# Kernel optimization log

Hardware: AMD Instinct MI355X
Metric: run time of the kernel (lower is better)

Reference implementation:

```python
import jax, jax.numpy as jnp
import numpy as np
from jax import lax

# quantization constants (from init_kwargs)
IN_SCALE = 0.05
IN_ZP = 128
W_SCALE = 0.02
W_ZP = 128
OUT_SCALE = 0.1
OUT_ZP = 0
PADDING = 1


def setup_inputs() -> dict:
    key = jax.random.key(0)
    k1, k2, k3 = jax.random.split(key, 3)
    x_float = jax.random.normal(k1, (8, 32, 512, 512), dtype=jnp.float32)
    weight = jax.random.randint(k2, (32, 32, 3, 3), 0, 256, dtype=jnp.int32)  # uint8-like
    bias = jax.random.randint(k3, (32,), 0, 100, dtype=jnp.int32)  # int32 accumulator bias
    return {"x_float": x_float, "weight": weight, "bias": bias}


def reference(x_float, weight, bias):
    # quantize input to uint8 range, then recenter
    x_q = jnp.round(x_float / IN_SCALE) + IN_ZP
    x_q = jnp.clip(x_q, 0, 255).astype(jnp.int32) - IN_ZP
    # recenter weights
    w_q = weight - W_ZP
    # integer conv emulated in float (NCHW, OIHW), 'same' padding=1
    y_int = lax.conv_general_dilated(
        x_q.astype(jnp.float32), w_q.astype(jnp.float32),
        window_strides=(1, 1), padding=[(PADDING, PADDING), (PADDING, PADDING)],
        dimension_numbers=("NCHW", "OIHW", "NCHW"),
    ).astype(jnp.int32)
    y_int = y_int + bias[None, :, None, None]
    # requantize + dequantize + relu (fused elementwise)
    scale_float = IN_SCALE * W_SCALE / OUT_SCALE
    y_q = jnp.clip(jnp.round(y_int.astype(jnp.float32) * scale_float), -127, 127).astype(jnp.int32)
    y = (y_q - OUT_ZP).astype(jnp.float32) * OUT_SCALE
    return jax.nn.relu(y)
```

## Files before the change

kernel.cpp:

```cpp
#include <hip/hip_runtime.h>


#define N_IMG 8
#define CIN   32
#define COUT  32
#define HD    512
#define WD    512
#define PH    514
#define PW    514
#define TH    8

typedef int intx4 __attribute__((ext_vector_type(4)));
typedef short short8 __attribute__((ext_vector_type(8)));
typedef float floatx4 __attribute__((ext_vector_type(4)));

#define XQ_BYTES ((size_t)N_IMG * PH * PW * CIN)
#define SLACK    256
#define WP_BYTES (6 * 32 * 64)
#define WS_NEED  (XQ_BYTES + SLACK + WP_BYTES)

__global__ __launch_bounds__(256) void quant8_kernel(const float* __restrict__ x,
                                                     unsigned char* __restrict__ xq) {
    const int gid = blockIdx.x * 256 + threadIdx.x;
    const int w = gid & (WD - 1);
    const int h = (gid >> 9) & (HD - 1);
    const int n = gid >> 18;
    const float* xp = x + ((size_t)n * CIN * HD + h) * WD + w;
    unsigned int pk[8];
#pragma unroll
    for (int c = 0; c < CIN; c += 4) {
        unsigned int b[4];
#pragma unroll
        for (int j = 0; j < 4; ++j) {
            float xv = xp[(size_t)(c + j) * (HD * WD)];
            float q = rintf(xv / 0.05f);
            q = fminf(fmaxf(q, -128.0f), 127.0f);
            b[j] = (unsigned int)(int)q & 0xffu;
        }
        pk[c >> 2] = b[0] | (b[1] << 8) | (b[2] << 16) | (b[3] << 24);
    }
    uint4* dst = (uint4*)(xq + (((size_t)n * PH + h + 1) * PW + (w + 1)) * CIN);
    dst[0] = make_uint4(pk[0], pk[1], pk[2], pk[3]);
    dst[1] = make_uint4(pk[4], pk[5], pk[6], pk[7]);
}

#define N_BORDER (N_IMG * 2052)
#define N_WP     (6 * 32 * 64)
__global__ __launch_bounds__(256) void aux8_kernel(const int* __restrict__ wq,
                                                   unsigned char* __restrict__ xq,
                                                   char* __restrict__ wp) {
    const int gid = blockIdx.x * 256 + threadIdx.x;
    if (gid < N_BORDER) {
        const int n = gid / 2052;
        const int p = gid - n * 2052;
        int h, w;
        if (p < 514)       { h = 0;   w = p; }
        else if (p < 1028) { h = 513; w = p - 514; }
        else { int q = p - 1028; h = 1 + (q >> 1); w = (q & 1) ? 513 : 0; }
        uint4* dst = (uint4*)(xq + (((size_t)n * PH + h) * PW + w) * CIN);
        uint4 z = make_uint4(0u, 0u, 0u, 0u);
        dst[0] = z; dst[1] = z;
    } else if (gid < N_BORDER + N_WP) {
        const int i = gid - N_BORDER;
        const int row  = i >> 6;
        const int k    = i & 63;
        const int khp  = row >> 5;
        const int cout = row & 31;
        const int kh   = khp >> 1;
        const int pr   = khp & 1;
        const int sel  = k >> 5;
        const int cin  = k & 31;
        const int kw   = pr * 2 + sel;
        int val = 0;
        if (kw < 3) val = wq[((cout * CIN + cin) * 3 + kh) * 3 + kw] - 128;
        wp[i] = (char)val;
    }
}

__global__ __launch_bounds__(256, 3) void conv8_kernel(const unsigned char* __restrict__ xq,
                                                       const char* __restrict__ wp,
                                                       const int* __restrict__ bias,
                                                       float* __restrict__ out) {
    const int tid  = threadIdx.x;
    const int lane = tid & 63;
    const int wave = tid >> 6;
    const int l15  = lane & 15;
    const int quad = lane >> 4;
    const int bx = blockIdx.x;
    const int by = blockIdx.y;
    const int n  = blockIdx.z;

    intx4 Af[3][2][2];
#pragma unroll
    for (int kh = 0; kh < 3; ++kh)
#pragma unroll
        for (int p = 0; p < 2; ++p)
#pragma unroll
            for (int hf = 0; hf < 2; ++hf)
                Af[kh][p][hf] = *(const intx4*)(wp + (((kh * 2 + p) * 32 + hf * 16 + l15) << 6) + quad * 16);

    int bi0[4], bi1[4];
#pragma unroll
    for (int r = 0; r < 4; ++r) { bi0[r] = bias[quad * 4 + r]; bi1[r] = bias[16 + quad * 4 + r]; }

    const int w0 = bx * 64 + wave * 16;
    const size_t rstride = (size_t)PW * CIN;
    const unsigned char* pbase = xq + (((size_t)n * PH + by * TH) * PW + (w0 + l15)) * CIN + quad * 16;

    intx4 Bf[10][2];
#pragma unroll
    for (int r = 0; r < 4; ++r)
#pragma unroll
        for (int p = 0; p < 2; ++p)
            Bf[r][p] = *(const intx4*)(pbase + r * rstride + p * 64);

#pragma unroll
    for (int it = 0; it < 4; ++it) {
        if (it < 3) {
#pragma unroll
            for (int r = 0; r < 2; ++r)
#pragma unroll
                for (int p = 0; p < 2; ++p)
                    Bf[2 * it + 4 + r][p] = *(const intx4*)(pbase + (2 * it + 4 + r) * rstride + p * 64);
        }
        intx4 acc[2][2];
#pragma unroll
        for (int o = 0; o < 2; ++o)
#pragma unroll
            for (int hf = 0; hf < 2; ++hf)
                acc[o][hf] = (intx4){0, 0, 0, 0};
#pragma unroll
        for (int o = 0; o < 2; ++o)
#pragma unroll
            for (int kh = 0; kh < 3; ++kh)
#pragma unroll
                for (int p = 0; p < 2; ++p) {
                    const intx4 b = Bf[2 * it + o + kh][p];
                    acc[o][0] = __builtin_amdgcn_mfma_i32_16x16x64_i8(Af[kh][p][0], b, acc[o][0], 0, 0, 0);
                    acc[o][1] = __builtin_amdgcn_mfma_i32_16x16x64_i8(Af[kh][p][1], b, acc[o][1], 0, 0, 0);
                }
#pragma unroll
        for (int o = 0; o < 2; ++o) {
            const int h = by * TH + 2 * it + o;
            float* op0 = out + (((size_t)n * COUT + quad * 4) * HD + h) * WD + w0 + l15;
            float* op1 = op0 + (size_t)16 * HD * WD;
#pragma unroll
            for (int r = 0; r < 4; ++r) {
                int v0 = acc[o][0][r] + bi0[r];
                float yq0 = rintf((float)v0 * 0.01f);
                yq0 = fminf(fmaxf(yq0, -127.f), 127.f);
                op0[(size_t)r * (HD * WD)] = fmaxf(yq0 * 0.1f, 0.f);
                int v1 = acc[o][1][r] + bi1[r];
                float yq1 = rintf((float)v1 * 0.01f);
                yq1 = fminf(fmaxf(yq1, -127.f), 127.f);
                op1[(size_t)r * (HD * WD)] = fmaxf(yq1 * 0.1f, 0.f);
            }
        }
    }
}

__launch_bounds__(256, 2)
__global__ void conv2d_int8_fused(const float* __restrict__ x,
                                  const int* __restrict__ wq,
                                  const int* __restrict__ bias,
                                  float* __restrict__ out)
{
    __shared__ unsigned short xs[10 * 66 * 32];
    __shared__ unsigned short ws[9 * 32 * 32];
    const int tid = threadIdx.x;
    const int bx = blockIdx.x, by = blockIdx.y, n = blockIdx.z;
    for (int i = tid; i < COUT * CIN * 9; i += 256) {
        int cout = i / 288, rem = i - cout * 288, cin = rem / 9, t = rem - cin * 9;
        float f = (float)(wq[i] - 128);
        ws[(t * 32 + cout) * 32 + cin] = (unsigned short)(__float_as_uint(f) >> 16);
    }
    const int h_base = by * TH - 1;
    const int w_base = bx * 64 - 1;
    for (int j = tid; j < CIN * 10 * 66; j += 256) {
        int c = j / 660, rem = j - c * 660, r = rem / 66, wc = rem - r * 66;
        int h = h_base + r, w = w_base + wc;
        float q = 0.0f;
        if ((unsigned)h < (unsigned)HD && (unsigned)w < (unsigned)WD) {
            float xv = x[((size_t)(n * CIN + c) * HD + h) * WD + w];
            q = rintf(xv / 0.05f);
            q = fminf(fmaxf(q, -128.0f), 127.0f);
        }
        unsigned short b = (unsigned short)(__float_as_uint(q) >> 16);
        int pix = r * 66 + wc;
        int grp = (c >> 3) ^ (pix & 3);
        xs[pix * 32 + (grp << 3) + (c & 7)] = b;
    }
    __syncthreads();
    const int lane = tid & 63, wave = tid >> 6;
    const int l15 = lane & 15, quad = lane >> 4;
    short8 bfrag[9][2];
#pragma unroll
    for (int t = 0; t < 9; ++t)
#pragma unroll
        for (int hf = 0; hf < 2; ++hf)
            bfrag[t][hf] = *(const short8*)&ws[(t * 32 + hf * 16 + l15) * 32 + quad * 8];
    const float b0 = (float)bias[l15];
    const float b1 = (float)bias[16 + l15];
    const int wseg = wave * 16;
    for (int hr = 0; hr < TH; ++hr) {
        floatx4 acc0 = {0.f, 0.f, 0.f, 0.f};
        floatx4 acc1 = {0.f, 0.f, 0.f, 0.f};
#pragma unroll
        for (int kh = 0; kh < 3; ++kh)
#pragma unroll
            for (int kw = 0; kw < 3; ++kw) {
                int pix = (hr + kh) * 66 + wseg + l15 + kw;
                int grp = quad ^ (pix & 3);
                short8 a = *(const short8*)&xs[pix * 32 + (grp << 3)];
                int t = kh * 3 + kw;
                acc0 = __builtin_amdgcn_mfma_f32_16x16x32_bf16(a, bfrag[t][0], acc0, 0, 0, 0);
                acc1 = __builtin_amdgcn_mfma_f32_16x16x32_bf16(a, bfrag[t][1], acc1, 0, 0, 0);
            }
        const int h_out = by * TH + hr;
        const int w_out0 = bx * 64 + wseg;
#pragma unroll
        for (int r = 0; r < 4; ++r) {
            int wo = w_out0 + quad * 4 + r;
            {
                float v = acc0[r] + b0;
                float yq = rintf(v * 0.01f);
                yq = fminf(fmaxf(yq, -127.f), 127.f);
                out[((size_t)(n * COUT + l15) * HD + h_out) * WD + wo] = fmaxf(yq * 0.1f, 0.f);
            }
            {
                float v = acc1[r] + b1;
                float yq = rintf(v * 0.01f);
                yq = fminf(fmaxf(yq, -127.f), 127.f);
                out[((size_t)(n * COUT + 16 + l15) * HD + h_out) * WD + wo] = fmaxf(yq * 0.1f, 0.f);
            }
        }
    }
}

extern "C" void kernel_launch(void* const* d_in, const int* in_sizes, int n_in,
                              void* d_out, int out_size, void* d_ws, size_t ws_size,
                              hipStream_t stream) {
    const float* x  = (const float*)d_in[0];
    const int*   wq = (const int*)d_in[1];
    const int*   bi = (const int*)d_in[2];
    float* out = (float*)d_out;

    if (ws_size >= WS_NEED) {
        unsigned char* xq = (unsigned char*)d_ws;
        char* wp = (char*)d_ws + XQ_BYTES + SLACK;
        aux8_kernel<<<(N_BORDER + N_WP + 255) / 256, 256, 0, stream>>>(wq, xq, wp);
        quant8_kernel<<<(N_IMG * HD * WD) / 256, 256, 0, stream>>>(x, xq);
        conv8_kernel<<<dim3(WD / 64, HD / TH, N_IMG), dim3(256), 0, stream>>>(xq, wp, bi, out);
    } else {
        conv2d_int8_fused<<<dim3(WD / 64, HD / TH, N_IMG), dim3(256), 0, stream>>>(x, wq, bi, out);
    }
}
```

Measured before the change: 527.1 us.

## Fuse input quantization and weight packing into single int8 conv kernel via LDS

Replaces the three-kernel pipeline (border/weight prep, global int8 quantization pass, conv) with one fused kernel. Each block quantizes its 10x68 halo tile of fp32 input straight into shared memory as int8 NHWC and builds the packed weights in LDS, then runs the same int8 MFMA conv reading B fragments from LDS. This removes the int8 intermediate write/read round trip through global memory and two launches. In exchange each block re-reads halo input (about 1.33x overlap) and redoes weight packing, and the strided fp32 channel loads may coalesce less well.

Result: slower. 640.4 us (+21.5%).

```diff
diff --git a/kernel.cpp b/kernel.cpp
--- a/kernel.cpp
+++ b/kernel.cpp
@@ -6,62 +6,27 @@
 #define COUT  32
 #define HD    512
 #define WD    512
-#define PH    514
-#define PW    514
 #define TH    8
+#define TW    64
+#define XROWS 10
+#define XCOLS 68
 
 typedef int intx4 __attribute__((ext_vector_type(4)));
-typedef short short8 __attribute__((ext_vector_type(8)));
-typedef float floatx4 __attribute__((ext_vector_type(4)));
 
-#define XQ_BYTES ((size_t)N_IMG * PH * PW * CIN)
-#define SLACK    256
-#define WP_BYTES (6 * 32 * 64)
-#define WS_NEED  (XQ_BYTES + SLACK + WP_BYTES)
+__global__ __launch_bounds__(256, 3) void conv8_fused(const float* __restrict__ x,
+                                                      const int* __restrict__ wq,
+                                                      const int* __restrict__ bias,
+                                                      float* __restrict__ out)
+{
+    __shared__ alignas(16) unsigned char xs[XROWS * XCOLS * CIN];
+    __shared__ alignas(16) char wp[6 * 32 * 64];
 
-__global__ __launch_bounds__(256) void quant8_kernel(const float* __restrict__ x,
-                                                     unsigned char* __restrict__ xq) {
-    const int gid = blockIdx.x * 256 + threadIdx.x;
-    const int w = gid & (WD - 1);
-    const int h = (gid >> 9) & (HD - 1);
-    const int n = gid >> 18;
-    const float* xp = x + ((size_t)n * CIN * HD + h) * WD + w;
-    unsigned int pk[8];
-#pragma unroll
-    for (int c = 0; c < CIN; c += 4) {
-        unsigned int b[4];
-#pragma unroll
-        for (int j = 0; j < 4; ++j) {
-            float xv = xp[(size_t)(c + j) * (HD * WD)];
-            float q = rintf(xv / 0.05f);
-            q = fminf(fmaxf(q, -128.0f), 127.0f);
-            b[j] = (unsigned int)(int)q & 0xffu;
-        }
-        pk[c >> 2] = b[0] | (b[1] << 8) | (b[2] << 16) | (b[3] << 24);
-    }
-    uint4* dst = (uint4*)(xq + (((size_t)n * PH + h + 1) * PW + (w + 1)) * CIN);
-    dst[0] = make_uint4(pk[0], pk[1], pk[2], pk[3]);
-    dst[1] = make_uint4(pk[4], pk[5], pk[6], pk[7]);
-}
+    const int tid = threadIdx.x;
+    const int bx = blockIdx.x;
+    const int by = blockIdx.y;
+    const int n  = blockIdx.z;
 
-#define N_BORDER (N_IMG * 2052)
-#define N_WP     (6 * 32 * 64)
-__global__ __launch_bounds__(256) void aux8_kernel(const int* __restrict__ wq,
-                                                   unsigned char* __restrict__ xq,
-                                                   char* __restrict__ wp) {
-    const int gid = blockIdx.x * 256 + threadIdx.x;
-    if (gid < N_BORDER) {
-        const int n = gid / 2052;
-        const int p = gid - n * 2052;
-        int h, w;
-        if (p < 514)       { h = 0;   w = p; }
-        else if (p < 1028) { h = 513; w = p - 514; }
-        else { int q = p - 1028; h = 1 + (q >> 1); w = (q & 1) ? 513 : 0; }
-        uint4* dst = (uint4*)(xq + (((size_t)n * PH + h) * PW + w) * CIN);
-        uint4 z = make_uint4(0u, 0u, 0u, 0u);
-        dst[0] = z; dst[1] = z;
-    } else if (gid < N_BORDER + N_WP) {
-        const int i = gid - N_BORDER;
+    for (int i = tid; i < 6 * 32 * 64; i += 256) {
         const int row  = i >> 6;
         const int k    = i & 63;
         const int khp  = row >> 5;
@@ -71,24 +36,46 @@
         const int sel  = k >> 5;
         const int cin  = k & 31;
         const int kw   = pr * 2 + sel;
-        int val = 0;
-        if (kw < 3) val = wq[((cout * CIN + cin) * 3 + kh) * 3 + kw] - 128;
-        wp[i] = (char)val;
+        int v = 0;
+        if (kw < 3) v = wq[((cout * CIN + cin) * 3 + kh) * 3 + kw] - 128;
+        wp[i] = (char)v;
     }
-}
 
-__global__ __launch_bounds__(256, 3) void conv8_kernel(const unsigned char* __restrict__ xq,
-                                                       const char* __restrict__ wp,
-                                                       const int* __restrict__ bias,
-                                                       float* __restrict__ out) {
-    const int tid  = threadIdx.x;
+    const int h0  = by * TH - 1;
+    const int wt0 = bx * TW - 1;
+    for (int i = tid; i < 2 * XROWS * XCOLS; i += 256) {
+        const int half = i / (XROWS * XCOLS);
+        const int rem  = i - half * (XROWS * XCOLS);
+        const int row  = rem / XCOLS;
+        const int pc   = rem - row * XCOLS;
+        const int h = h0 + row;
+        const int w = wt0 + pc;
+        unsigned int pk[4] = {0u, 0u, 0u, 0u};
+        if ((unsigned)h < (unsigned)HD && (unsigned)w < (unsigned)WD) {
+            const float* xp = x + ((size_t)(n * CIN + half * 16) * HD + h) * WD + w;
+#pragma unroll
+            for (int c4 = 0; c4 < 4; ++c4) {
+                unsigned int b[4];
+#pragma unroll
+                for (int j = 0; j < 4; ++j) {
+                    float xv = xp[(size_t)(c4 * 4 + j) * (HD * WD)];
+                    float q = rintf(xv / 0.05f);
+                    q = fminf(fmaxf(q, -128.0f), 127.0f);
+                    b[j] = (unsigned int)(int)q & 0xffu;
+                }
+                pk[c4] = b[0] | (b[1] << 8) | (b[2] << 16) | (b[3] << 24);
+            }
+        }
+        *(uint4*)(xs + (size_t)(row * XCOLS + pc) * CIN + half * 16) =
+            make_uint4(pk[0], pk[1], pk[2], pk[3]);
+    }
+
+    __syncthreads();
+
     const int lane = tid & 63;
     const int wave = tid >> 6;
     const int l15  = lane & 15;
     const int quad = lane >> 4;
-    const int bx = blockIdx.x;
-    const int by = blockIdx.y;
-    const int n  = blockIdx.z;
 
     intx4 Af[3][2][2];
 #pragma unroll
@@ -103,46 +90,40 @@
 #pragma unroll
     for (int r = 0; r < 4; ++r) { bi0[r] = bias[quad * 4 + r]; bi1[r] = bias[16 + quad * 4 + r]; }
 
-    const int w0 = bx * 64 + wave * 16;
-    const size_t rstride = (size_t)PW * CIN;
-    const unsigned char* pbase = xq + (((size_t)n * PH + by * TH) * PW + (w0 + l15)) * CIN + quad * 16;
-
-    intx4 Bf[10][2];
-#pragma unroll
-    for (int r = 0; r < 4; ++r)
-#pragma unroll
-        for (int p = 0; p < 2; ++p)
-            Bf[r][p] = *(const intx4*)(pbase + r * rstride + p * 64);
+    const int wseg = wave * 16;
+    const unsigned char* bbase = xs + (size_t)(wseg + l15) * CIN + quad * 16;
 
 #pragma unroll
     for (int it = 0; it < 4; ++it) {
-        if (it < 3) {
+        intx4 Bw[4][2];
 #pragma unroll
-            for (int r = 0; r < 2; ++r)
+        for (int r = 0; r < 4; ++r)
 #pragma unroll
-                for (int p = 0; p < 2; ++p)
-                    Bf[2 * it + 4 + r][p] = *(const intx4*)(pbase + (2 * it + 4 + r) * rstride + p * 64);
-        }
+            for (int p = 0; p < 2; ++p)
+                Bw[r][p] = *(const intx4*)(bbase + (size_t)((2 * it + r) * XCOLS) * CIN + p * 64);
+
         intx4 acc[2][2];
 #pragma unroll
         for (int o = 0; o < 2; ++o)
 #pragma unroll
             for (int hf = 0; hf < 2; ++hf)
                 acc[o][hf] = (intx4){0, 0, 0, 0};
+
 #pragma unroll
         for (int o = 0; o < 2; ++o)
 #pragma unroll
             for (int kh = 0; kh < 3; ++kh)
 #pragma unroll
                 for (int p = 0; p < 2; ++p) {
-                    const intx4 b = Bf[2 * it + o + kh][p];
+                    const intx4 b = Bw[o + kh][p];
                     acc[o][0] = __builtin_amdgcn_mfma_i32_16x16x64_i8(Af[kh][p][0], b, acc[o][0], 0, 0, 0);
                     acc[o][1] = __builtin_amdgcn_mfma_i32_16x16x64_i8(Af[kh][p][1], b, acc[o][1], 0, 0, 0);
                 }
+
 #pragma unroll
         for (int o = 0; o < 2; ++o) {
             const int h = by * TH + 2 * it + o;
-            float* op0 = out + (((size_t)n * COUT + quad * 4) * HD + h) * WD + w0 + l15;
+            float* op0 = out + (((size_t)n * COUT + quad * 4) * HD + h) * WD + bx * TW + wseg + l15;
             float* op1 = op0 + (size_t)16 * HD * WD;
 #pragma unroll
             for (int r = 0; r < 4; ++r) {
@@ -159,84 +140,6 @@
     }
 }
 
-__launch_bounds__(256, 2)
-__global__ void conv2d_int8_fused(const float* __restrict__ x,
-                                  const int* __restrict__ wq,
-                                  const int* __restrict__ bias,
-                                  float* __restrict__ out)
-{
-    __shared__ unsigned short xs[10 * 66 * 32];
-    __shared__ unsigned short ws[9 * 32 * 32];
-    const int tid = threadIdx.x;
-    const int bx = blockIdx.x, by = blockIdx.y, n = blockIdx.z;
-    for (int i = tid; i < COUT * CIN * 9; i += 256) {
-        int cout = i / 288, rem = i - cout * 288, cin = rem / 9, t = rem - cin * 9;
-        float f = (float)(wq[i] - 128);
-        ws[(t * 32 + cout) * 32 + cin] = (unsigned short)(__float_as_uint(f) >> 16);
-    }
-    const int h_base = by * TH - 1;
-    const int w_base = bx * 64 - 1;
-    for (int j = tid; j < CIN * 10 * 66; j += 256) {
-        int c = j / 660, rem = j - c * 660, r = rem / 66, wc = rem - r * 66;
-        int h = h_base + r, w = w_base + wc;
-        float q = 0.0f;
-        if ((unsigned)h < (unsigned)HD && (unsigned)w < (unsigned)WD) {
-            float xv = x[((size_t)(n * CIN + c) * HD + h) * WD + w];
-            q = rintf(xv / 0.05f);
-            q = fminf(fmaxf(q, -128.0f), 127.0f);
-        }
-        unsigned short b = (unsigned short)(__float_as_uint(q) >> 16);
-        int pix = r * 66 + wc;
-        int grp = (c >> 3) ^ (pix & 3);
-        xs[pix * 32 + (grp << 3) + (c & 7)] = b;
-    }
-    __syncthreads();
-    const int lane = tid & 63, wave = tid >> 6;
-    const int l15 = lane & 15, quad = lane >> 4;
-    short8 bfrag[9][2];
-#pragma unroll
-    for (int t = 0; t < 9; ++t)
-#pragma unroll
-        for (int hf = 0; hf < 2; ++hf)
-            bfrag[t][hf] = *(const short8*)&ws[(t * 32 + hf * 16 + l15) * 32 + quad * 8];
-    const float b0 = (float)bias[l15];
-    const float b1 = (float)bias[16 + l15];
-    const int wseg = wave * 16;
-    for (int hr = 0; hr < TH; ++hr) {
-        floatx4 acc0 = {0.f, 0.f, 0.f, 0.f};
-        floatx4 acc1 = {0.f, 0.f, 0.f, 0.f};
-#pragma unroll
-        for (int kh = 0; kh < 3; ++kh)
-#pragma unroll
-            for (int kw = 0; kw < 3; ++kw) {
-                int pix = (hr + kh) * 66 + wseg + l15 + kw;
-                int grp = quad ^ (pix & 3);
-                short8 a = *(const short8*)&xs[pix * 32 + (grp << 3)];
-                int t = kh * 3 + kw;
-                acc0 = __builtin_amdgcn_mfma_f32_16x16x32_bf16(a, bfrag[t][0], acc0, 0, 0, 0);
-                acc1 = __builtin_amdgcn_mfma_f32_16x16x32_bf16(a, bfrag[t][1], acc1, 0, 0, 0);
-            }
-        const int h_out = by * TH + hr;
-        const int w_out0 = bx * 64 + wseg;
-#pragma unroll
-        for (int r = 0; r < 4; ++r) {
-            int wo = w_out0 + quad * 4 + r;
-            {
-                float v = acc0[r] + b0;
-                float yq = rintf(v * 0.01f);
-                yq = fminf(fmaxf(yq, -127.f), 127.f);
-                out[((size_t)(n * COUT + l15) * HD + h_out) * WD + wo] = fmaxf(yq * 0.1f, 0.f);
-            }
-            {
-                float v = acc1[r] + b1;
-                float yq = rintf(v * 0.01f);
-                yq = fminf(fmaxf(yq, -127.f), 127.f);
-                out[((size_t)(n * COUT + 16 + l15) * HD + h_out) * WD + wo] = fmaxf(yq * 0.1f, 0.f);
-            }
-        }
-    }
-}
-
 extern "C" void kernel_launch(void* const* d_in, const int* in_sizes, int n_in,
                               void* d_out, int out_size, void* d_ws, size_t ws_size,
                               hipStream_t stream) {
@@ -244,14 +147,7 @@
     const int*   wq = (const int*)d_in[1];
     const int*   bi = (const int*)d_in[2];
     float* out = (float*)d_out;
+    (void)d_ws; (void)ws_size;
 
-    if (ws_size >= WS_NEED) {
-        unsigned char* xq = (unsigned char*)d_ws;
-        char* wp = (char*)d_ws + XQ_BYTES + SLACK;
-        aux8_kernel<<<(N_BORDER + N_WP + 255) / 256, 256, 0, stream>>>(wq, xq, wp);
-        quant8_kernel<<<(N_IMG * HD * WD) / 256, 256, 0, stream>>>(x, xq);
-        conv8_kernel<<<dim3(WD / 64, HD / TH, N_IMG), dim3(256), 0, stream>>>(xq, wp, bi, out);
-    } else {
-        conv2d_int8_fused<<<dim3(WD / 64, HD / TH, N_IMG), dim3(256), 0, stream>>>(x, wq, bi, out);
-    }
+    conv8_fused<<<dim3(WD / TW, HD / TH, N_IMG), dim3(256), 0, stream>>>(x, wq, bi, out);
 }
```
